# Kernel optimization log

Hardware: AMD Instinct MI355X
Metric: run time of the kernel (lower is better)

Reference implementation:

```python
import jax, jax.numpy as jnp
import numpy as np

N_U, N_I, E = 500000, 50000, 1000000
H, C = 4, 32  # heads, per-head channels


def _seg_softmax(e, dst, n_dst):
    # e: [E, H] edge scores, softmax over edges sharing the same destination
    m = jax.ops.segment_max(e, dst, num_segments=n_dst)
    ex = jnp.exp(e - m[dst])
    s = jax.ops.segment_sum(ex, dst, num_segments=n_dst)
    return ex / (s[dst] + 1e-16)


def _gatv2(xl, xr, src, dst, att, bias, n_dst, edge_feat=None):
    # GATv2 bipartite message passing (PyG semantics, no self-loops for bipartite).
    # xl: [N_src,H,C] transformed source, xr: [N_dst,H,C] transformed destination
    h = xl[src] + xr[dst]                      # [E,H,C] gather + add
    if edge_feat is not None:
        h = h + edge_feat                      # [E,H,C]
    e = jnp.sum(jax.nn.leaky_relu(h, 0.2) * att, axis=-1)   # [E,H]
    alpha = _seg_softmax(e, dst, n_dst)                      # [E,H]
    out = jax.ops.segment_sum(alpha[..., None] * xl[src], dst, num_segments=n_dst)
    return out.reshape(n_dst, H * C) + bias    # concat heads + bias


def setup_inputs() -> dict:
    key = jax.random.key(0)
    ks = iter(jax.random.split(key, 32))
    p = lambda *s: jax.random.normal(next(ks), s, dtype=jnp.float32) * 0.05
    inp = {
        "customer_x": jax.random.normal(next(ks), (N_U, 101), dtype=jnp.float32),
        "fund_x": jax.random.normal(next(ks), (N_I, 1), dtype=jnp.float32),
        "edge_attr": jax.random.uniform(next(ks), (E, 3), dtype=jnp.float32),
        "edge_src": jax.random.randint(next(ks), (E,), 0, N_U),
        "edge_dst": jax.random.randint(next(ks), (E,), 0, N_I),
        # input projections
        "user_W": p(101, 32), "user_b": jnp.zeros((32,), jnp.float32),
        "item_W": p(1, 32),   "item_b": jnp.zeros((32,), jnp.float32),
        # conv1: GATv2Conv((32,32), 32, heads=4, edge_dim=3)
        "c1_Wl": p(32, H * C), "c1_bl": jnp.zeros((H * C,), jnp.float32),
        "c1_Wr": p(32, H * C), "c1_br": jnp.zeros((H * C,), jnp.float32),
        "c1_We": p(3, H * C),
        "c1_att": p(H, C), "c1_bias": jnp.zeros((H * C,), jnp.float32),
        # conv2: GATv2Conv((128,32), 32, heads=4), called without edge_attr
        "c2_Wl": p(H * C, H * C), "c2_bl": jnp.zeros((H * C,), jnp.float32),
        "c2_Wr": p(32, H * C),    "c2_br": jnp.zeros((H * C,), jnp.float32),
        "c2_att": p(H, C), "c2_bias": jnp.zeros((H * C,), jnp.float32),
        # classifier MLP: 128 -> 64 -> 1
        "cls_W1": p(128, 64), "cls_b1": jnp.zeros((64,), jnp.float32),
        "cls_W2": p(64, 1),   "cls_b2": jnp.zeros((1,), jnp.float32),
    }
    return inp


def reference(customer_x, fund_x, edge_attr, edge_src, edge_dst,
              user_W, user_b, item_W, item_b,
              c1_Wl, c1_bl, c1_Wr, c1_br, c1_We, c1_att, c1_bias,
              c2_Wl, c2_bl, c2_Wr, c2_br, c2_att, c2_bias,
              cls_W1, cls_b1, cls_W2, cls_b2):
    user_x = customer_x @ user_W + user_b            # [N_U,32]
    item_x = fund_x @ item_W + item_b                # [N_I,32]
    # conv1: customer -> fund (dst = fund)
    xl1 = (user_x @ c1_Wl + c1_bl).reshape(N_U, H, C)
    xr1 = (item_x @ c1_Wr + c1_br).reshape(N_I, H, C)
    ef1 = (edge_attr @ c1_We).reshape(E, H, C)
    item_h = jax.nn.relu(_gatv2(xl1, xr1, edge_src, edge_dst, c1_att, c1_bias, N_I, ef1))
    # conv2: fund -> customer (edge_index flipped, no edge_attr)
    xl2 = (item_h @ c2_Wl + c2_bl).reshape(N_I, H, C)
    xr2 = (user_x @ c2_Wr + c2_br).reshape(N_U, H, C)
    user_h = _gatv2(xl2, xr2, edge_dst, edge_src, c2_att, c2_bias, N_U)  # [N_U,128]
    # anomaly classifier
    hid = jax.nn.relu(user_h @ cls_W1 + cls_b1)
    scores = jax.nn.sigmoid(hid @ cls_W2 + cls_b2)   # [N_U,1]
    return scores
```

## Files before the change

kernel.cpp:

```cpp
#include <hip/hip_runtime.h>
#include <cstdint>
#include <cstddef>

#define NU 500000
#define NI 50000
#define NE 1000000
#define HC 128
#define NH 4

typedef __attribute__((ext_vector_type(8))) short bf16x8;
typedef __attribute__((ext_vector_type(4))) float f32x4;

union frag_u { bf16x8 v; unsigned int u[4]; };

__device__ __forceinline__ unsigned int pack_bf2(float x, float y) {
    unsigned int xb = __float_as_uint(x);
    unsigned int yb = __float_as_uint(y);
    xb += 0x7fffu + ((xb >> 16) & 1u);
    yb += 0x7fffu + ((yb >> 16) & 1u);
    return (xb >> 16) | (yb & 0xffff0000u);
}
__device__ __forceinline__ float2 unpack_bf2(unsigned int v) {
    return make_float2(__uint_as_float(v << 16),
                       __uint_as_float(v & 0xffff0000u));
}
__device__ __forceinline__ unsigned short pack_bf1(float x) {
    unsigned int b = __float_as_uint(x);
    b += 0x7fffu + ((b >> 16) & 1u);
    return (unsigned short)(b >> 16);
}

__device__ __forceinline__ float head_reduce(float p) {
    p += __shfl_xor(p, 8, 16);
    p += __shfl_xor(p, 4, 16);
    p += __shfl_xor(p, 2, 16);
    p += __shfl_xor(p, 1, 16);
    return p;
}

__global__ void wprep(const float* __restrict__ user_W, const float* __restrict__ user_b,
                      const float* __restrict__ c1_Wl, const float* __restrict__ c1_bl,
                      const float* __restrict__ c2_Wr, const float* __restrict__ c2_br,
                      const float* __restrict__ c2_Wl, unsigned short* __restrict__ Bp)
{
    const int t = blockIdx.x * 256 + threadIdx.x;
    const int mat = t >> 14;
    const int k = (t >> 7) & 127;
    const int n = t & 127;
    float val = 0.f;
    if (mat == 2) {
        val = c2_Wl[k * 128 + n];
    } else {
        const float* W2 = mat ? c2_Wr : c1_Wl;
        if (k < 101) {
            for (int q = 0; q < 32; ++q) val = fmaf(user_W[k * 32 + q], W2[q * 128 + n], val);
        } else if (k == 101) {
            for (int q = 0; q < 32; ++q) val = fmaf(user_b[q], W2[q * 128 + n], val);
            val += (mat ? c2_br : c1_bl)[n];
        }
    }
    const int fi = (mat * 8 + (n >> 4)) * 4 + (k >> 5);
    const int lane_ = (n & 15) + ((k >> 3) & 3) * 16;
    Bp[(size_t)fi * 512 + lane_ * 8 + (k & 7)] = pack_bf1(val);
}

__global__ void w1prep(const float* __restrict__ W1, unsigned short* __restrict__ Bp1)
{
    const int t = blockIdx.x * 256 + threadIdx.x;
    const int k = t >> 6;
    const int n = t & 63;
    const float val = W1[k * 64 + n];
    const int fi = (n >> 4) * 4 + (k >> 5);
    const int lane_ = (n & 15) + ((k >> 3) & 3) * 16;
    Bp1[(size_t)fi * 512 + lane_ * 8 + (k & 7)] = pack_bf1(val);
}

__global__ void wvbb_prep(const float* __restrict__ item_W, const float* __restrict__ item_b,
                          const float* __restrict__ c1_Wr, const float* __restrict__ c1_br,
                          float* __restrict__ wvbb)
{
    const int j = threadIdx.x;
    if (j >= 128) return;
    float wv = 0.f, bb = 0.f;
    for (int q = 0; q < 32; ++q) {
        wv = fmaf(item_W[q], c1_Wr[q * 128 + j], wv);
        bb = fmaf(item_b[q], c1_Wr[q * 128 + j], bb);
    }
    wvbb[j] = wv;
    wvbb[128 + j] = bb + c1_br[j];
}

__global__ void xr1_outer(const float* __restrict__ fund_x, const float* __restrict__ wvbb,
                          float* __restrict__ C, int n)
{
    for (int i = blockIdx.x * blockDim.x + threadIdx.x; i < n;
         i += gridDim.x * blockDim.x) {
        const int row = i >> 7, j = i & 127;
        C[i] = fmaf(fund_x[row], wvbb[j], wvbb[128 + j]);
    }
}

__global__ __launch_bounds__(256)
void mfma_user(const float* __restrict__ cx, const unsigned short* __restrict__ Bp,
               unsigned short* __restrict__ outL, unsigned short* __restrict__ outR, int M)
{
    __shared__ float xs[64 * 108];

    const int tid = threadIdx.x;
    const int lane = tid & 63;
    const int wid = tid >> 6;
    const int rowblk = blockIdx.x * 64;
    const int rows = min(64, M - rowblk);

    const float* src = cx + (size_t)rowblk * 101;
    const int total = rows * 101;
    for (int i = tid; i < total; i += 256) {
        const int r = i / 101;
        const int c = i - r * 101;
        xs[r * 108 + c] = src[i];
    }
    __syncthreads();

    const int rowbase = wid * 16;
    if (rowbase >= rows) return;
    const int row = lane & 15;
    const int chunk = lane >> 4;
    const float* rowp = xs + (rowbase + row) * 108;

    frag_u a[4];
    #pragma unroll
    for (int ks = 0; ks < 3; ++ks) {
        const int kb = ks * 32 + chunk * 8;
        const float4 p = *(const float4*)(rowp + kb);
        const float4 q = *(const float4*)(rowp + kb + 4);
        a[ks].u[0] = pack_bf2(p.x, p.y);
        a[ks].u[1] = pack_bf2(p.z, p.w);
        a[ks].u[2] = pack_bf2(q.x, q.y);
        a[ks].u[3] = pack_bf2(q.z, q.w);
    }
    {
        float v0 = 0.f, v1 = 0.f, v2 = 0.f, v3 = 0.f, v4 = 0.f, v5 = 0.f;
        if (chunk == 0) {
            const float4 p = *(const float4*)(rowp + 96);
            v0 = p.x; v1 = p.y; v2 = p.z; v3 = p.w;
            v4 = rowp[100];
            v5 = 1.0f;
        }
        a[3].u[0] = pack_bf2(v0, v1);
        a[3].u[1] = pack_bf2(v2, v3);
        a[3].u[2] = pack_bf2(v4, v5);
        a[3].u[3] = 0u;
    }

    unsigned short* xpo = (unsigned short*)(xs + (size_t)wid * 16 * 108);

    const bf16x8* bfr = (const bf16x8*)Bp;
    #pragma unroll
    for (int mat = 0; mat < 2; ++mat) {
        unsigned short* outp = mat ? outR : outL;
        #pragma unroll
        for (int nf = 0; nf < 8; ++nf) {
            f32x4 acc = {0.f, 0.f, 0.f, 0.f};
            const int fi = (mat * 8 + nf) * 4;
            acc = __builtin_amdgcn_mfma_f32_16x16x32_bf16(a[0].v, bfr[(fi + 0) * 64 + lane], acc, 0, 0, 0);
            acc = __builtin_amdgcn_mfma_f32_16x16x32_bf16(a[1].v, bfr[(fi + 1) * 64 + lane], acc, 0, 0, 0);
            acc = __builtin_amdgcn_mfma_f32_16x16x32_bf16(a[2].v, bfr[(fi + 2) * 64 + lane], acc, 0, 0, 0);
            acc = __builtin_amdgcn_mfma_f32_16x16x32_bf16(a[3].v, bfr[(fi + 3) * 64 + lane], acc, 0, 0, 0);
            const int col = nf * 16 + row;
            #pragma unroll
            for (int j = 0; j < 4; ++j)
                xpo[(chunk * 4 + j) * 140 + col] = pack_bf1(acc[j]);
        }
        #pragma unroll
        for (int i = 0; i < 4; ++i) {
            const int r = i * 4 + chunk;
            const bf16x8 v = *(const bf16x8*)&xpo[r * 140 + row * 8];
            *(bf16x8*)(outp + (size_t)(rowblk + rowbase + r) * 128 + row * 8) = v;
        }
    }
}

__global__ __launch_bounds__(256)
void mfma_xl2(const float* __restrict__ X, const unsigned short* __restrict__ Bp,
              const float* __restrict__ bias, unsigned short* __restrict__ outp, int M)
{
    const int lane = threadIdx.x & 63;
    const int wt = (blockIdx.x * blockDim.x + threadIdx.x) >> 6;
    const int rowbase = wt * 16;
    if (rowbase >= M) return;
    const int chunk = lane >> 4;
    const float* rowp = X + (size_t)(rowbase + (lane & 15)) * 128;

    frag_u a[4];
    #pragma unroll
    for (int ks = 0; ks < 4; ++ks) {
        const int kb = ks * 32 + chunk * 8;
        const float4 p = *(const float4*)(rowp + kb);
        const float4 q = *(const float4*)(rowp + kb + 4);
        a[ks].u[0] = pack_bf2(p.x, p.y);
        a[ks].u[1] = pack_bf2(p.z, p.w);
        a[ks].u[2] = pack_bf2(q.x, q.y);
        a[ks].u[3] = pack_bf2(q.z, q.w);
    }

    const bf16x8* bfr = (const bf16x8*)Bp;
    #pragma unroll
    for (int nf = 0; nf < 8; ++nf) {
        f32x4 acc = {0.f, 0.f, 0.f, 0.f};
        const int fi = (16 + nf) * 4;
        acc = __builtin_amdgcn_mfma_f32_16x16x32_bf16(a[0].v, bfr[(fi + 0) * 64 + lane], acc, 0, 0, 0);
        acc = __builtin_amdgcn_mfma_f32_16x16x32_bf16(a[1].v, bfr[(fi + 1) * 64 + lane], acc, 0, 0, 0);
        acc = __builtin_amdgcn_mfma_f32_16x16x32_bf16(a[2].v, bfr[(fi + 2) * 64 + lane], acc, 0, 0, 0);
        acc = __builtin_amdgcn_mfma_f32_16x16x32_bf16(a[3].v, bfr[(fi + 3) * 64 + lane], acc, 0, 0, 0);
        const int col = nf * 16 + (lane & 15);
        const float bv = bias[col];
        #pragma unroll
        for (int j = 0; j < 4; ++j)
            outp[(size_t)(rowbase + chunk * 4 + j) * 128 + col] = pack_bf1(acc[j] + bv);
    }
}

__global__ void hist_rank(const int* __restrict__ src, const int* __restrict__ dst,
                          int* __restrict__ cntU, int* __restrict__ cntI,
                          int* __restrict__ rankU, int* __restrict__ rankI, int E)
{
    for (int i = blockIdx.x * blockDim.x + threadIdx.x; i < E;
         i += gridDim.x * blockDim.x) {
        rankU[i] = atomicAdd(&cntU[src[i]], 1);
        rankI[i] = atomicAdd(&cntI[dst[i]], 1);
    }
}

__global__ void scan_blocks(const int* __restrict__ in, int* __restrict__ out,
                            int* __restrict__ blockSums, int n)
{
    __shared__ int lds[256];
    const int tid = threadIdx.x;
    const int base = blockIdx.x * 1024 + tid * 4;
    int v[4];
    #pragma unroll
    for (int j = 0; j < 4; ++j) { int idx = base + j; v[j] = (idx < n) ? in[idx] : 0; }
    int t = v[0] + v[1] + v[2] + v[3];
    lds[tid] = t;
    __syncthreads();
    for (int off = 1; off < 256; off <<= 1) {
        int x = (tid >= off) ? lds[tid - off] : 0;
        __syncthreads();
        lds[tid] += x;
        __syncthreads();
    }
    int excl = lds[tid] - t;
    if (tid == 255 && blockSums) blockSums[blockIdx.x] = lds[255];
    int run = excl;
    #pragma unroll
    for (int j = 0; j < 4; ++j) {
        int idx = base + j;
        if (idx < n) out[idx] = run;
        run += v[j];
    }
}

__global__ void scan_add(int* __restrict__ out, const int* __restrict__ bss, int n)
{
    const int add = bss[blockIdx.x];
    const int base = blockIdx.x * 1024 + threadIdx.x * 4;
    #pragma unroll
    for (int j = 0; j < 4; ++j) { int idx = base + j; if (idx < n) out[idx] += add; }
}

__global__ void scatter_ranked(const int* __restrict__ src, const int* __restrict__ dst,
                               const float* __restrict__ eattr,
                               const int* __restrict__ offU, const int* __restrict__ offI,
                               const int* __restrict__ rankU, const int* __restrict__ rankI,
                               int* __restrict__ sFund, uint4* __restrict__ sE1, int E)
{
    for (int i = blockIdx.x * blockDim.x + threadIdx.x; i < E;
         i += gridDim.x * blockDim.x) {
        const int s = src[i];
        const int d = dst[i];
        const float a0 = eattr[3 * (size_t)i];
        const float a1 = eattr[3 * (size_t)i + 1];
        const float a2 = eattr[3 * (size_t)i + 2];
        const int p1 = offI[d] + rankI[i];
        const int p2 = offU[s] + rankU[i];
        sE1[p1] = make_uint4((unsigned int)s, __float_as_uint(a0),
                             __float_as_uint(a1), __float_as_uint(a2));
        sFund[p2] = d;
    }
}

__device__ __forceinline__ void conv1_edge(uint4 e, unsigned int vbits, float2 vr,
                                           float2 av, float2 w0, float2 w1, float2 w2,
                                           float& acc0, float& acc1, float& s)
{
    const float2 vl = unpack_bf2(vbits);
    const float e0 = __uint_as_float(e.y);
    const float e1 = __uint_as_float(e.z);
    const float e2 = __uint_as_float(e.w);
    float h0 = vl.x + vr.x + e0 * w0.x + e1 * w1.x + e2 * w2.x;
    float h1 = vl.y + vr.y + e0 * w0.y + e1 * w1.y + e2 * w2.y;
    h0 = h0 > 0.f ? h0 : 0.2f * h0;
    h1 = h1 > 0.f ? h1 : 0.2f * h1;
    const float p = head_reduce(h0 * av.x + h1 * av.y);
    const float ex = __expf(p);
    acc0 = fmaf(ex, vl.x, acc0);
    acc1 = fmaf(ex, vl.y, acc1);
    s += ex;
}

__global__ void conv1_fused(const unsigned int* __restrict__ xl,
                            const float* __restrict__ xr,
                            const int* __restrict__ offI, const int* __restrict__ cnt,
                            const uint4* __restrict__ sE,
                            const float* __restrict__ We, const float* __restrict__ att,
                            const float* __restrict__ bias,
                            float* __restrict__ outF, int ndst)
{
    const int tid = threadIdx.x;
    const int lane = tid & 63;
    const int wid = tid >> 6;
    const int d = blockIdx.x * 4 + wid;
    if (d >= ndst) return;

    const int ch = lane * 2;
    const float2 av = *(const float2*)(att + ch);
    const float2 w0 = *(const float2*)(We + ch);
    const float2 w1 = *(const float2*)(We + HC + ch);
    const float2 w2 = *(const float2*)(We + 2 * HC + ch);
    const float2 bv = *(const float2*)(bias + ch);
    const float2 vr = *(const float2*)(xr + (size_t)d * HC + ch);

    const int start = offI[d];
    const int end = start + cnt[d];

    float acc0 = 0.f, acc1 = 0.f, s = 0.f;
    int pos = start;
    for (; pos + 8 <= end; pos += 8) {
        uint4 e[8];
        unsigned int v[8];
        #pragma unroll
        for (int j = 0; j < 8; ++j) e[j] = sE[pos + j];
        #pragma unroll
        for (int j = 0; j < 8; ++j) v[j] = xl[(size_t)e[j].x * 64 + lane];
        #pragma unroll
        for (int j = 0; j < 8; ++j)
            conv1_edge(e[j], v[j], vr, av, w0, w1, w2, acc0, acc1, s);
    }
    for (; pos + 4 <= end; pos += 4) {
        uint4 e[4];
        unsigned int v[4];
        #pragma unroll
        for (int j = 0; j < 4; ++j) e[j] = sE[pos + j];
        #pragma unroll
        for (int j = 0; j < 4; ++j) v[j] = xl[(size_t)e[j].x * 64 + lane];
        #pragma unroll
        for (int j = 0; j < 4; ++j)
            conv1_edge(e[j], v[j], vr, av, w0, w1, w2, acc0, acc1, s);
    }
    for (; pos < end; ++pos) {
        const uint4 e = sE[pos];
        const unsigned int v = xl[(size_t)e.x * 64 + lane];
        conv1_edge(e, v, vr, av, w0, w1, w2, acc0, acc1, s);
    }
    const float inv = 1.f / (s + 1e-16f);
    const float o0 = fmaxf(acc0 * inv + bv.x, 0.f);
    const float o1 = fmaxf(acc1 * inv + bv.y, 0.f);
    *(float2*)(outF + (size_t)d * HC + ch) = make_float2(o0, o1);
}

__device__ __forceinline__ void conv2_edge(unsigned int vbits, float2 vr, float2 av,
                                           float& acc0, float& acc1, float& s)
{
    const float2 vl = unpack_bf2(vbits);
    float h0 = vl.x + vr.x;
    float h1 = vl.y + vr.y;
    h0 = h0 > 0.f ? h0 : 0.2f * h0;
    h1 = h1 > 0.f ? h1 : 0.2f * h1;
    const float p = head_reduce(h0 * av.x + h1 * av.y);
    const float ex = __expf(p);
    acc0 = fmaf(ex, vl.x, acc0);
    acc1 = fmaf(ex, vl.y, acc1);
    s += ex;
}

__global__ __launch_bounds__(256)
void conv2_cls(const unsigned int* __restrict__ xl2,
               const unsigned int* __restrict__ xr2,
               const int* __restrict__ offU, const int* __restrict__ cnt,
               const int* __restrict__ sFund,
               const float* __restrict__ att, const float* __restrict__ cbias,
               const unsigned short* __restrict__ Bp1,
               const float* __restrict__ b1, const float* __restrict__ W2,
               const float* __restrict__ b2,
               float* __restrict__ out, int nusr)
{
    __shared__ unsigned short xs[4][16][136];

    const int lane = threadIdx.x & 63;
    const int wid = threadIdx.x >> 6;
    const int wt = (blockIdx.x * blockDim.x + threadIdx.x) >> 6;
    const int u0 = wt * 16;
    if (u0 >= nusr) return;

    const int ch = lane * 2;
    const float2 av = *(const float2*)(att + ch);
    const float2 bv = *(const float2*)(cbias + ch);

    int so = 0, ctv = 0;
    if (lane < 16) {
        so = offU[u0 + lane];
        ctv = cnt[u0 + lane];
    }
    const int eo = so + ctv;
    const int S = __builtin_amdgcn_readlane(so, 0);
    const int E = __builtin_amdgcn_readlane(eo, 15);

    int u = 0;
    int end_u = __builtin_amdgcn_readlane(eo, 0);
    unsigned int vrb_next = xr2[(size_t)(u0 + 1) * 64 + lane];
    float2 vr = unpack_bf2(xr2[(size_t)u0 * 64 + lane]);
    float acc0 = 0.f, acc1 = 0.f, s = 0.f;

    #define FINALIZE() {                                                        \
        const float inv = 1.f / (s + 1e-16f);                                   \
        *(unsigned int*)&xs[wid][u][ch] = pack_bf2(acc0 * inv + bv.x,           \
                                                   acc1 * inv + bv.y);          \
        acc0 = acc1 = s = 0.f;                                                  \
        ++u;                                                                    \
        if (u < 16) {                                                           \
            end_u = __builtin_amdgcn_readlane(eo, u);                           \
            vr = unpack_bf2(vrb_next);                                          \
            if (u + 1 < 16) vrb_next = xr2[(size_t)(u0 + u + 1) * 64 + lane];   \
        }                                                                       \
    }

    int pos = S;
    while (pos < E) {
        const int f0 = sFund[pos];
        const int f1 = (pos + 1 < E) ? sFund[pos + 1] : f0;
        const int f2 = (pos + 2 < E) ? sFund[pos + 2] : f0;
        const int f3 = (pos + 3 < E) ? sFund[pos + 3] : f0;
        const unsigned int v0 = xl2[(size_t)f0 * 64 + lane];
        const unsigned int v1 = xl2[(size_t)f1 * 64 + lane];
        const unsigned int v2 = xl2[(size_t)f2 * 64 + lane];
        const unsigned int v3 = xl2[(size_t)f3 * 64 + lane];

        while (pos == end_u) FINALIZE();
        conv2_edge(v0, vr, av, acc0, acc1, s);
        if (pos + 1 < E) {
            while (pos + 1 == end_u) FINALIZE();
            conv2_edge(v1, vr, av, acc0, acc1, s);
        }
        if (pos + 2 < E) {
            while (pos + 2 == end_u) FINALIZE();
            conv2_edge(v2, vr, av, acc0, acc1, s);
        }
        if (pos + 3 < E) {
            while (pos + 3 == end_u) FINALIZE();
            conv2_edge(v3, vr, av, acc0, acc1, s);
        }
        pos += 4;
    }
    while (u < 16) FINALIZE();
    #undef FINALIZE

    const int row = lane & 15;
    const int chunk = lane >> 4;
    bf16x8 a[4];
    #pragma unroll
    for (int ks = 0; ks < 4; ++ks)
        a[ks] = *(const bf16x8*)&xs[wid][row][ks * 32 + chunk * 8];

    const bf16x8* bfr = (const bf16x8*)Bp1;
    float racc[4] = {0.f, 0.f, 0.f, 0.f};
    #pragma unroll
    for (int g = 0; g < 4; ++g) {
        f32x4 acc = {0.f, 0.f, 0.f, 0.f};
        const int fi = g * 4;
        acc = __builtin_amdgcn_mfma_f32_16x16x32_bf16(a[0], bfr[(fi + 0) * 64 + lane], acc, 0, 0, 0);
        acc = __builtin_amdgcn_mfma_f32_16x16x32_bf16(a[1], bfr[(fi + 1) * 64 + lane], acc, 0, 0, 0);
        acc = __builtin_amdgcn_mfma_f32_16x16x32_bf16(a[2], bfr[(fi + 2) * 64 + lane], acc, 0, 0, 0);
        acc = __builtin_amdgcn_mfma_f32_16x16x32_bf16(a[3], bfr[(fi + 3) * 64 + lane], acc, 0, 0, 0);
        const int col = g * 16 + row;
        const float b1v = b1[col];
        const float w2v = W2[col];
        #pragma unroll
        for (int j = 0; j < 4; ++j)
            racc[j] = fmaf(fmaxf(acc[j] + b1v, 0.f), w2v, racc[j]);
    }
    #pragma unroll
    for (int j = 0; j < 4; ++j) {
        racc[j] += __shfl_xor(racc[j], 1, 16);
        racc[j] += __shfl_xor(racc[j], 2, 16);
        racc[j] += __shfl_xor(racc[j], 4, 16);
        racc[j] += __shfl_xor(racc[j], 8, 16);
    }
    if (row == 0) {
        const float b2v = b2[0];
        #pragma unroll
        for (int j = 0; j < 4; ++j) {
            const int r = u0 + chunk * 4 + j;
            if (r < nusr) out[r] = 1.f / (1.f + expf(-(racc[j] + b2v)));
        }
    }
}

extern "C" void kernel_launch(void* const* d_in, const int* in_sizes, int n_in,
                              void* d_out, int out_size, void* d_ws, size_t ws_size,
                              hipStream_t stream)
{
    const float* customer_x = (const float*)d_in[0];
    const float* fund_x     = (const float*)d_in[1];
    const float* edge_attr  = (const float*)d_in[2];
    const int*   edge_src   = (const int*)d_in[3];
    const int*   edge_dst   = (const int*)d_in[4];
    const float* user_W = (const float*)d_in[5];
    const float* user_b = (const float*)d_in[6];
    const float* item_W = (const float*)d_in[7];
    const float* item_b = (const float*)d_in[8];
    const float* c1_Wl  = (const float*)d_in[9];
    const float* c1_bl  = (const float*)d_in[10];
    const float* c1_Wr  = (const float*)d_in[11];
    const float* c1_br  = (const float*)d_in[12];
    const float* c1_We  = (const float*)d_in[13];
    const float* c1_att = (const float*)d_in[14];
    const float* c1_bias= (const float*)d_in[15];
    const float* c2_Wl  = (const float*)d_in[16];
    const float* c2_bl  = (const float*)d_in[17];
    const float* c2_Wr  = (const float*)d_in[18];
    const float* c2_br  = (const float*)d_in[19];
    const float* c2_att = (const float*)d_in[20];
    const float* c2_bias= (const float*)d_in[21];
    const float* cls_W1 = (const float*)d_in[22];
    const float* cls_b1 = (const float*)d_in[23];
    const float* cls_W2 = (const float*)d_in[24];
    const float* cls_b2 = (const float*)d_in[25];
    float* out = (float*)d_out;

    float* ws = (float*)d_ws;
    size_t off = 0;
    unsigned short* B1 = (unsigned short*)(ws + off); off += (size_t)NU * 64;
    unsigned short* B2 = (unsigned short*)(ws + off); off += (size_t)NU * 64;
    float* C = ws + off; off += (size_t)NI * HC;
    float* F = ws + off; off += (size_t)NI * HC;
    unsigned short* G = (unsigned short*)(ws + off); off += (size_t)NI * 64;
    int* cnt1  = (int*)(ws + off); off += NI;
    int* off1  = (int*)(ws + off); off += NI;
    int* cnt2  = (int*)(ws + off); off += NU;
    int* off2  = (int*)(ws + off); off += NU;
    int* bs    = (int*)(ws + off); off += 1024;
    int* bss   = (int*)(ws + off); off += 1024;
    uint4* sE1 = (uint4*)(ws + off); off += (size_t)NE * 4;
    int* sFund = (int*)(ws + off); off += NE;
    int* rankU = (int*)(ws + off); off += NE;
    int* rankI = (int*)(ws + off); off += NE;
    unsigned short* Bp = (unsigned short*)(ws + off); off += 12288 + 256;
    unsigned short* Bp1 = (unsigned short*)(ws + off); off += 4096 + 256;
    float* wvbb = ws + off; off += 256;

    hipMemsetAsync(cnt1, 0, NI * sizeof(int), stream);
    hipMemsetAsync(cnt2, 0, NU * sizeof(int), stream);

    hist_rank<<<1024, 256, 0, stream>>>(edge_src, edge_dst, cnt2, cnt1,
                                        rankU, rankI, NE);
    const int nb1 = (NI + 1023) / 1024;
    const int nb2 = (NU + 1023) / 1024;
    scan_blocks<<<nb1, 256, 0, stream>>>(cnt1, off1, bs, NI);
    scan_blocks<<<1,   256, 0, stream>>>(bs, bss, nullptr, nb1);
    scan_add<<<nb1, 256, 0, stream>>>(off1, bss, NI);
    scan_blocks<<<nb2, 256, 0, stream>>>(cnt2, off2, bs, NU);
    scan_blocks<<<1,   256, 0, stream>>>(bs, bss, nullptr, nb2);
    scan_add<<<nb2, 256, 0, stream>>>(off2, bss, NU);
    scatter_ranked<<<2048, 256, 0, stream>>>(edge_src, edge_dst, edge_attr,
                                             off2, off1, rankU, rankI,
                                             sFund, sE1, NE);

    wprep<<<192, 256, 0, stream>>>(user_W, user_b, c1_Wl, c1_bl,
                                   c2_Wr, c2_br, c2_Wl, Bp);
    w1prep<<<32, 256, 0, stream>>>(cls_W1, Bp1);
    wvbb_prep<<<1, 128, 0, stream>>>(item_W, item_b, c1_Wr, c1_br, wvbb);

    xr1_outer<<<2048, 256, 0, stream>>>(fund_x, wvbb, C, NI * HC);

    mfma_user<<<(NU + 63) / 64, 256, 0, stream>>>(customer_x, Bp, B1, B2, NU);

    conv1_fused<<<NI / 4, 256, 0, stream>>>((const unsigned int*)B1, C, off1, cnt1, sE1,
                                            c1_We, c1_att, c1_bias, F, NI);

    mfma_xl2<<<(NI / 16 + 3) / 4, 256, 0, stream>>>(F, Bp, c2_bl, G, NI);

    const int waves2 = (NU + 15) / 16;
    conv2_cls<<<(waves2 + 3) / 4, 256, 0, stream>>>(
        (const unsigned int*)G, (const unsigned int*)B2, off2, cnt2, sFund,
        c2_att, c2_bias, Bp1, cls_b1, cls_W2, cls_b2, out, NU);
}
```

Baseline: 553.7 us.

## Stage user rows as bf16 in LDS and compute two row groups per wave

mfma_user now converts customer_x to packed bf16 while loading it into shared memory. Each block covers 128 rows and each wave computes two 16-row groups, so every B fragment loaded from global memory feeds two MFMAs. pack_bf2 now uses the hardware v_cvt_pk_bf16_f32 instruction instead of integer rounding. The cost is that global loads become scalar and strided per pair, and each wave holds more registers.

```diff
diff --git a/kernel.cpp b/kernel.cpp
--- a/kernel.cpp
+++ b/kernel.cpp
@@ -14,11 +14,9 @@
 union frag_u { bf16x8 v; unsigned int u[4]; };
 
 __device__ __forceinline__ unsigned int pack_bf2(float x, float y) {
-    unsigned int xb = __float_as_uint(x);
-    unsigned int yb = __float_as_uint(y);
-    xb += 0x7fffu + ((xb >> 16) & 1u);
-    yb += 0x7fffu + ((yb >> 16) & 1u);
-    return (xb >> 16) | (yb & 0xffff0000u);
+    unsigned int r;
+    asm("v_cvt_pk_bf16_f32 %0, %1, %2" : "=v"(r) : "v"(x), "v"(y));
+    return r;
 }
 __device__ __forceinline__ float2 unpack_bf2(unsigned int v) {
     return make_float2(__uint_as_float(v << 16),
@@ -104,55 +102,46 @@
 void mfma_user(const float* __restrict__ cx, const unsigned short* __restrict__ Bp,
                unsigned short* __restrict__ outL, unsigned short* __restrict__ outR, int M)
 {
-    __shared__ float xs[64 * 108];
+    __shared__ unsigned int xsb[128 * 68];
 
     const int tid = threadIdx.x;
     const int lane = tid & 63;
     const int wid = tid >> 6;
-    const int rowblk = blockIdx.x * 64;
-    const int rows = min(64, M - rowblk);
-
-    const float* src = cx + (size_t)rowblk * 101;
-    const int total = rows * 101;
-    for (int i = tid; i < total; i += 256) {
-        const int r = i / 101;
-        const int c = i - r * 101;
-        xs[r * 108 + c] = src[i];
+    const int rowblk = blockIdx.x * 128;
+    const int rows = min(128, M - rowblk);
+
+    const int totalPairs = rows * 68;
+    for (int i = tid; i < totalPairs; i += 256) {
+        const int r = i / 68;
+        const int c = i - r * 68;
+        unsigned int v = 0u;
+        if (c < 50) {
+            const float x0 = cx[(size_t)(rowblk + r) * 101 + 2 * c];
+            const float x1 = cx[(size_t)(rowblk + r) * 101 + 2 * c + 1];
+            v = pack_bf2(x0, x1);
+        } else if (c == 50) {
+            v = pack_bf2(cx[(size_t)(rowblk + r) * 101 + 100], 1.0f);
+        }
+        xsb[r * 68 + c] = v;
     }
     __syncthreads();
 
-    const int rowbase = wid * 16;
-    if (rowbase >= rows) return;
+    const int wrow = wid * 32;
+    if (wrow >= rows) return;
     const int row = lane & 15;
     const int chunk = lane >> 4;
-    const float* rowp = xs + (rowbase + row) * 108;
-
-    frag_u a[4];
-    #pragma unroll
-    for (int ks = 0; ks < 3; ++ks) {
-        const int kb = ks * 32 + chunk * 8;
-        const float4 p = *(const float4*)(rowp + kb);
-        const float4 q = *(const float4*)(rowp + kb + 4);
-        a[ks].u[0] = pack_bf2(p.x, p.y);
-        a[ks].u[1] = pack_bf2(p.z, p.w);
-        a[ks].u[2] = pack_bf2(q.x, q.y);
-        a[ks].u[3] = pack_bf2(q.z, q.w);
-    }
-    {
-        float v0 = 0.f, v1 = 0.f, v2 = 0.f, v3 = 0.f, v4 = 0.f, v5 = 0.f;
-        if (chunk == 0) {
-            const float4 p = *(const float4*)(rowp + 96);
-            v0 = p.x; v1 = p.y; v2 = p.z; v3 = p.w;
-            v4 = rowp[100];
-            v5 = 1.0f;
-        }
-        a[3].u[0] = pack_bf2(v0, v1);
-        a[3].u[1] = pack_bf2(v2, v3);
-        a[3].u[2] = pack_bf2(v4, v5);
-        a[3].u[3] = 0u;
-    }
-
-    unsigned short* xpo = (unsigned short*)(xs + (size_t)wid * 16 * 108);
+
+    const unsigned short* xbase = (const unsigned short*)xsb;
+    bf16x8 ag[2][4];
+    #pragma unroll
+    for (int rg = 0; rg < 2; ++rg) {
+        const int rr = wrow + rg * 16 + row;
+        #pragma unroll
+        for (int ks = 0; ks < 4; ++ks)
+            ag[rg][ks] = *(const bf16x8*)&xbase[rr * 136 + ks * 32 + chunk * 8];
+    }
+
+    unsigned short* xp = (unsigned short*)&xsb[wid * 32 * 68];
 
     const bf16x8* bfr = (const bf16x8*)Bp;
     #pragma unroll
@@ -160,22 +149,29 @@
         unsigned short* outp = mat ? outR : outL;
         #pragma unroll
         for (int nf = 0; nf < 8; ++nf) {
-            f32x4 acc = {0.f, 0.f, 0.f, 0.f};
             const int fi = (mat * 8 + nf) * 4;
-            acc = __builtin_amdgcn_mfma_f32_16x16x32_bf16(a[0].v, bfr[(fi + 0) * 64 + lane], acc, 0, 0, 0);
-            acc = __builtin_amdgcn_mfma_f32_16x16x32_bf16(a[1].v, bfr[(fi + 1) * 64 + lane], acc, 0, 0, 0);
-            acc = __builtin_amdgcn_mfma_f32_16x16x32_bf16(a[2].v, bfr[(fi + 2) * 64 + lane], acc, 0, 0, 0);
-            acc = __builtin_amdgcn_mfma_f32_16x16x32_bf16(a[3].v, bfr[(fi + 3) * 64 + lane], acc, 0, 0, 0);
-            const int col = nf * 16 + row;
+            const bf16x8 b0 = bfr[(fi + 0) * 64 + lane];
+            const bf16x8 b1 = bfr[(fi + 1) * 64 + lane];
+            const bf16x8 b2 = bfr[(fi + 2) * 64 + lane];
+            const bf16x8 b3 = bfr[(fi + 3) * 64 + lane];
             #pragma unroll
-            for (int j = 0; j < 4; ++j)
-                xpo[(chunk * 4 + j) * 140 + col] = pack_bf1(acc[j]);
-        }
-        #pragma unroll
-        for (int i = 0; i < 4; ++i) {
-            const int r = i * 4 + chunk;
-            const bf16x8 v = *(const bf16x8*)&xpo[r * 140 + row * 8];
-            *(bf16x8*)(outp + (size_t)(rowblk + rowbase + r) * 128 + row * 8) = v;
+            for (int rg = 0; rg < 2; ++rg) {
+                f32x4 acc = {0.f, 0.f, 0.f, 0.f};
+                acc = __builtin_amdgcn_mfma_f32_16x16x32_bf16(ag[rg][0], b0, acc, 0, 0, 0);
+                acc = __builtin_amdgcn_mfma_f32_16x16x32_bf16(ag[rg][1], b1, acc, 0, 0, 0);
+                acc = __builtin_amdgcn_mfma_f32_16x16x32_bf16(ag[rg][2], b2, acc, 0, 0, 0);
+                acc = __builtin_amdgcn_mfma_f32_16x16x32_bf16(ag[rg][3], b3, acc, 0, 0, 0);
+                const int col = nf * 16 + row;
+                #pragma unroll
+                for (int j = 0; j < 4; ++j)
+                    xp[(rg * 16 + chunk * 4 + j) * 136 + col] = pack_bf1(acc[j]);
+            }
+        }
+        #pragma unroll
+        for (int i = 0; i < 8; ++i) {
+            const int lr = i * 4 + chunk;
+            const bf16x8 v = *(const bf16x8*)&xp[lr * 136 + row * 8];
+            *(bf16x8*)(outp + (size_t)(rowblk + wrow + lr) * 128 + row * 8) = v;
         }
     }
 }
@@ -582,7 +578,7 @@
 
     xr1_outer<<<2048, 256, 0, stream>>>(fund_x, wvbb, C, NI * HC);
 
-    mfma_user<<<(NU + 63) / 64, 256, 0, stream>>>(customer_x, Bp, B1, B2, NU);
+    mfma_user<<<(NU + 127) / 128, 256, 0, stream>>>(customer_x, Bp, B1, B2, NU);
 
     conv1_fused<<<NI / 4, 256, 0, stream>>>((const unsigned int*)B1, C, off1, cnt1, sE1,
                                             c1_We, c1_att, c1_bias, F, NI);
```

Result: slower. 625.9 us (+13.1%).
